# Kernel optimization log

Hardware: AMD Instinct MI355X
Metric: run time of the kernel (lower is better)

## Reference

```python
import jax, jax.numpy as jnp
import numpy as np
import math

B, T, D = 64, 128, 512
ALPHA = 20.0


def setup_inputs() -> dict:
    key = jax.random.key(0)
    k1, k2 = jax.random.split(key)
    x = jax.random.normal(k1, (B, T, D), dtype=jnp.float32)
    # Per-timestep fresh LSTMCell weights: uniform(-stdv, stdv) + tiled identity,
    # matching CellPro's re-initialization each step (stdv = 1/sqrt(1024)).
    stdv = 1.0 / math.sqrt(1024.0)
    eye4 = jnp.tile(jnp.eye(D, dtype=jnp.float32), (4, 1))  # [4D, D]
    w_ih = jax.random.uniform(k2, (T, 4 * D, D), dtype=jnp.float32,
                              minval=-stdv, maxval=stdv) + eye4[None]
    # Note: w_hh is also a parameter in the original, but h0 = 0 so it never
    # contributes to the output (gates = x @ w_ih^T + 0 @ w_hh^T). Omitted.
    return {"x": x, "w_ih": w_ih}


def reference(x, w_ih):
    # gates[b,t,:] = x[b,t,:] @ w_ih[t].T   (zero initial hidden state)
    gates = jnp.einsum('btd,tkd->btk', x, w_ih)  # [B, T, 4D]
    i, f, g, o = jnp.split(gates, 4, axis=-1)    # PyTorch LSTM gate order i,f,g,o
    c = jax.nn.sigmoid(i) * jnp.tanh(g)          # c' = f*c0 + i*g with c0 = 0
    h = jax.nn.sigmoid(o) * jnp.tanh(c)          # h' = o * tanh(c')
    return jax.nn.softmax(ALPHA * h, axis=-1)    # [B, T, D]
```

## Files before the change

kernel.cpp:

```cpp
#include <hip/hip_runtime.h>
#include <hip/hip_bf16.h>


#define B_ 64
#define T_ 128
#define D_ 512

typedef float f32x4_t __attribute__((ext_vector_type(4)));
typedef __bf16 bf16x8_t __attribute__((ext_vector_type(8)));
typedef unsigned short u16x8_t __attribute__((ext_vector_type(8)));
typedef unsigned short u16x4_t __attribute__((ext_vector_type(4)));

#define SWZ(r) ((unsigned)(((r) & 7) << 4))

__device__ __forceinline__ void cvt8(float4 a, float4 b, u16x8_t& hi, u16x8_t& lo) {
  float f[8] = {a.x, a.y, a.z, a.w, b.x, b.y, b.z, b.w};
#pragma unroll
  for (int j = 0; j < 8; ++j) {
    __bf16 h = (__bf16)f[j];
    hi[j] = __builtin_bit_cast(unsigned short, h);
    float r = f[j] - (float)h;
    lo[j] = __builtin_bit_cast(unsigned short, (__bf16)r);
  }
}

__device__ __forceinline__ void cvt4(float4 v, u16x4_t& hi, u16x4_t& lo) {
  float f[4] = {v.x, v.y, v.z, v.w};
#pragma unroll
  for (int j = 0; j < 4; ++j) {
    __bf16 h = (__bf16)f[j];
    hi[j] = __builtin_bit_cast(unsigned short, h);
    float r = f[j] - (float)h;
    lo[j] = __builtin_bit_cast(unsigned short, (__bf16)r);
  }
}

__device__ __forceinline__ f32x4_t mfma16(u16x8_t a, u16x8_t b, f32x4_t c) {
  return __builtin_amdgcn_mfma_f32_16x16x32_bf16(
      __builtin_bit_cast(bf16x8_t, a), __builtin_bit_cast(bf16x8_t, b), c, 0, 0, 0);
}

__device__ __forceinline__ float sigmoid_f(float v) { return 1.0f / (1.0f + __expf(-v)); }
__device__ __forceinline__ float tanh_f(float v) { return 1.0f - 2.0f / (__expf(2.0f * v) + 1.0f); }

__global__ __launch_bounds__(256, 2) void lstm_gates_kernel(
    const float* __restrict__ x, const float* __restrict__ w, float* __restrict__ out) {
  __shared__ char lds[2][16384];
  const int lane = threadIdx.x & 63;
  const int wv = threadIdx.x >> 6;
  const int bid = blockIdx.x;
  const int work = (bid & 7) * 128 + (bid >> 3);
  const int t = work >> 3;
  const int d0 = (work & 7) << 6;

  const int c = lane & 15;
  const int kg = lane >> 4;

  const int kl = lane * 4;
  const unsigned wst = (unsigned)(((kl >> 5) & 7) * 128);
  const unsigned wlow = (unsigned)((((kl >> 3) & 3) * 16) + ((kl & 4) << 1));
  unsigned wa_hi[4], wa_lo[4];
#pragma unroll
  for (int i = 0; i < 4; ++i) {
    const int rl = wv * 4 + i;
    wa_hi[i] = (unsigned)(rl * 1024) + wst + (wlow ^ SWZ(rl));
    wa_lo[i] = (unsigned)(rl * 1024) + wst + ((wlow + 64) ^ SWZ(rl));
  }
  const unsigned q_hi = ((unsigned)(kg * 16)) ^ SWZ(c);
  const unsigned q_lo = ((unsigned)(kg * 16 + 64)) ^ SWZ(c);
  const unsigned rbase = (unsigned)(c * 1024);

  const int grow[3] = {0, 1024, 1536};
  const char* wt = (const char*)w + ((size_t)t << 22) + (size_t)d0 * 2048;

  f32x4_t acc[12];
#pragma unroll
  for (int s = 0; s < 12; ++s) acc[s] = (f32x4_t){0.f, 0.f, 0.f, 0.f};

  u16x8_t xh[8], xl[8];
  float4 rs0[4], rs1[4];

#define LOADX(KH)                                                                      \
  do {                                                                                 \
    const float* xr_ = x + (((size_t)(wv * 16 + c) * T_ + t) << 9) + (KH) * 256 + kg * 8; \
    _Pragma("unroll") for (int st_ = 0; st_ < 8; ++st_) {                              \
      float4 a_ = *(const float4*)(xr_ + st_ * 32);                                    \
      float4 b_ = *(const float4*)(xr_ + st_ * 32 + 4);                                \
      cvt8(a_, b_, xh[st_], xl[st_]);                                                  \
    }                                                                                  \
  } while (0)

#define WOFF(SS)                                                                        \
  ((size_t)(grow[((SS) % 12) >> 2] + (((SS) % 12) & 3) * 16 + wv * 4) * 2048 +          \
   (size_t)((SS) / 12) * 1024)

#define ISSUE(SS, RS)                                                                   \
  do {                                                                                  \
    const char* gb_ = wt + WOFF(SS) + lane * 16;                                        \
    _Pragma("unroll") for (int i_ = 0; i_ < 4; ++i_)                                    \
        RS[i_] = *(const float4*)(gb_ + (size_t)i_ * 2048);                             \
  } while (0)

#define WRITE(SS, RS)                                                                   \
  do {                                                                                  \
    char* lb_ = &lds[(SS) & 1][0];                                                      \
    _Pragma("unroll") for (int i_ = 0; i_ < 4; ++i_) {                                  \
      u16x4_t h_, l_;                                                                   \
      cvt4(RS[i_], h_, l_);                                                             \
      *(u16x4_t*)(lb_ + wa_hi[i_]) = h_;                                                \
      *(u16x4_t*)(lb_ + wa_lo[i_]) = l_;                                                \
    }                                                                                   \
  } while (0)

#define BARRIER asm volatile("s_waitcnt lgkmcnt(0)\n\ts_barrier" ::: "memory")

#define COMPUTE(SS)                                                                     \
  do {                                                                                  \
    const char* lb_ = &lds[(SS) & 1][0];                                                \
    _Pragma("unroll") for (int st_ = 0; st_ < 8; ++st_) {                               \
      u16x8_t wh_ = *(const u16x8_t*)(lb_ + rbase + st_ * 128 + q_hi);                  \
      u16x8_t wl_ = *(const u16x8_t*)(lb_ + rbase + st_ * 128 + q_lo);                  \
      acc[(SS) % 12] = mfma16(xh[st_], wh_, acc[(SS) % 12]);                            \
      acc[(SS) % 12] = mfma16(xh[st_], wl_, acc[(SS) % 12]);                            \
      acc[(SS) % 12] = mfma16(xl[st_], wh_, acc[(SS) % 12]);                            \
    }                                                                                   \
  } while (0)

#define STEP(SS, RS)                        \
  WRITE(SS, RS);                            \
  if ((SS) + 2 < 24) ISSUE((SS) + 2, RS);   \
  BARRIER;                                  \
  COMPUTE(SS)

  LOADX(0);
  ISSUE(0, rs0);
  ISSUE(1, rs1);

  STEP(0, rs0);  STEP(1, rs1);  STEP(2, rs0);  STEP(3, rs1);
  STEP(4, rs0);  STEP(5, rs1);  STEP(6, rs0);  STEP(7, rs1);
  STEP(8, rs0);  STEP(9, rs1);  STEP(10, rs0); STEP(11, rs1);
  LOADX(1);
  STEP(12, rs0); STEP(13, rs1); STEP(14, rs0); STEP(15, rs1);
  STEP(16, rs0); STEP(17, rs1); STEP(18, rs0); STEP(19, rs1);
  STEP(20, rs0); STEP(21, rs1); STEP(22, rs0); STEP(23, rs1);

#undef STEP
#undef COMPUTE
#undef WRITE
#undef ISSUE
#undef WOFF
#undef LOADX

#pragma unroll
  for (int cg = 0; cg < 4; ++cg) {
#pragma unroll
    for (int j = 0; j < 4; ++j) {
      float iv = acc[cg][j];
      float gv = acc[4 + cg][j];
      float ov = acc[8 + cg][j];
      float cc = sigmoid_f(iv) * tanh_f(gv);
      float h = sigmoid_f(ov) * tanh_f(cc);
      int b = wv * 16 + kg * 4 + j;
      out[(((size_t)b * T_ + t) << 9) + d0 + cg * 16 + c] = h;
    }
  }
}

__global__ __launch_bounds__(256) void softmax_kernel(float* __restrict__ io) {
  const int lane = threadIdx.x & 63;
  const int row = blockIdx.x * 4 + (threadIdx.x >> 6);
  float* p = io + ((size_t)row << 9);
  float4 v0 = *(const float4*)(p + lane * 4);
  float4 v1 = *(const float4*)(p + 256 + lane * 4);
  float l[8] = {20.f * v0.x, 20.f * v0.y, 20.f * v0.z, 20.f * v0.w,
                20.f * v1.x, 20.f * v1.y, 20.f * v1.z, 20.f * v1.w};
  float m = l[0];
#pragma unroll
  for (int j = 1; j < 8; ++j) m = fmaxf(m, l[j]);
#pragma unroll
  for (int o = 32; o > 0; o >>= 1) m = fmaxf(m, __shfl_xor(m, o, 64));
  float e[8], s = 0.f;
#pragma unroll
  for (int j = 0; j < 8; ++j) {
    e[j] = __expf(l[j] - m);
    s += e[j];
  }
#pragma unroll
  for (int o = 32; o > 0; o >>= 1) s += __shfl_xor(s, o, 64);
  float inv = 1.0f / s;
  float4 o0 = {e[0] * inv, e[1] * inv, e[2] * inv, e[3] * inv};
  float4 o1 = {e[4] * inv, e[5] * inv, e[6] * inv, e[7] * inv};
  *(float4*)(p + lane * 4) = o0;
  *(float4*)(p + 256 + lane * 4) = o1;
}

extern "C" void kernel_launch(void* const* d_in, const int* in_sizes, int n_in,
                              void* d_out, int out_size, void* d_ws, size_t ws_size,
                              hipStream_t stream) {
  const float* x = (const float*)d_in[0];
  const float* w = (const float*)d_in[1];
  float* out = (float*)d_out;
  lstm_gates_kernel<<<T_ * 8, 256, 0, stream>>>(x, w, out);
  softmax_kernel<<<(B_ * T_) / 4, 256, 0, stream>>>(out);
}
```

Baseline: 98.37 us.

## Reorder K/gate loop to shrink accumulators from twelve to three

Changes the step order so that each column group's three gates (i, g, o) are accumulated over the full K before moving on. Only three accumulator tiles are live instead of twelve, and the epilogue runs and stores per column group. This lowers register pressure, which may help occupancy or avoid spills. In exchange, the x fragments are reloaded and reconverted from global memory eight times per block instead of twice, adding global loads and conversion ALU work.

```diff
diff --git a/kernel.cpp b/kernel.cpp
--- a/kernel.cpp
+++ b/kernel.cpp
@@ -73,57 +73,57 @@
   const int grow[3] = {0, 1024, 1536};
   const char* wt = (const char*)w + ((size_t)t << 22) + (size_t)d0 * 2048;
 
-  f32x4_t acc[12];
-#pragma unroll
-  for (int s = 0; s < 12; ++s) acc[s] = (f32x4_t){0.f, 0.f, 0.f, 0.f};
+  f32x4_t acc[3];
+#pragma unroll
+  for (int g = 0; g < 3; ++g) acc[g] = (f32x4_t){0.f, 0.f, 0.f, 0.f};
 
   u16x8_t xh[8], xl[8];
   float4 rs0[4], rs1[4];
 
-#define LOADX(KH)                                                                      \
-  do {                                                                                 \
+#define LOADX(KH)                                                                         \
+  do {                                                                                    \
     const float* xr_ = x + (((size_t)(wv * 16 + c) * T_ + t) << 9) + (KH) * 256 + kg * 8; \
-    _Pragma("unroll") for (int st_ = 0; st_ < 8; ++st_) {                              \
-      float4 a_ = *(const float4*)(xr_ + st_ * 32);                                    \
-      float4 b_ = *(const float4*)(xr_ + st_ * 32 + 4);                                \
-      cvt8(a_, b_, xh[st_], xl[st_]);                                                  \
-    }                                                                                  \
-  } while (0)
-
-#define WOFF(SS)                                                                        \
-  ((size_t)(grow[((SS) % 12) >> 2] + (((SS) % 12) & 3) * 16 + wv * 4) * 2048 +          \
-   (size_t)((SS) / 12) * 1024)
-
-#define ISSUE(SS, RS)                                                                   \
-  do {                                                                                  \
-    const char* gb_ = wt + WOFF(SS) + lane * 16;                                        \
-    _Pragma("unroll") for (int i_ = 0; i_ < 4; ++i_)                                    \
-        RS[i_] = *(const float4*)(gb_ + (size_t)i_ * 2048);                             \
-  } while (0)
-
-#define WRITE(SS, RS)                                                                   \
-  do {                                                                                  \
-    char* lb_ = &lds[(SS) & 1][0];                                                      \
-    _Pragma("unroll") for (int i_ = 0; i_ < 4; ++i_) {                                  \
-      u16x4_t h_, l_;                                                                   \
-      cvt4(RS[i_], h_, l_);                                                             \
-      *(u16x4_t*)(lb_ + wa_hi[i_]) = h_;                                                \
-      *(u16x4_t*)(lb_ + wa_lo[i_]) = l_;                                                \
-    }                                                                                   \
+    _Pragma("unroll") for (int st_ = 0; st_ < 8; ++st_) {                                 \
+      float4 a_ = *(const float4*)(xr_ + st_ * 32);                                       \
+      float4 b_ = *(const float4*)(xr_ + st_ * 32 + 4);                                   \
+      cvt8(a_, b_, xh[st_], xl[st_]);                                                     \
+    }                                                                                     \
+  } while (0)
+
+#define WOFF(SS)                                                                \
+  ((size_t)(grow[(SS) % 3] + ((SS) / 6) * 16 + wv * 4) * 2048 +                 \
+   (size_t)(((SS) / 3) & 1) * 1024)
+
+#define ISSUE(SS, RS)                                                           \
+  do {                                                                          \
+    const char* gb_ = wt + WOFF(SS) + lane * 16;                                \
+    _Pragma("unroll") for (int i_ = 0; i_ < 4; ++i_)                            \
+        RS[i_] = *(const float4*)(gb_ + (size_t)i_ * 2048);                     \
+  } while (0)
+
+#define WRITE(SS, RS)                                                           \
+  do {                                                                          \
+    char* lb_ = &lds[(SS) & 1][0];                                              \
+    _Pragma("unroll") for (int i_ = 0; i_ < 4; ++i_) {                          \
+      u16x4_t h_, l_;                                                           \
+      cvt4(RS[i_], h_, l_);                                                     \
+      *(u16x4_t*)(lb_ + wa_hi[i_]) = h_;                                        \
+      *(u16x4_t*)(lb_ + wa_lo[i_]) = l_;                                        \
+    }                                                                           \
   } while (0)
 
 #define BARRIER asm volatile("s_waitcnt lgkmcnt(0)\n\ts_barrier" ::: "memory")
 
-#define COMPUTE(SS)                                                                     \
-  do {                                                                                  \
-    const char* lb_ = &lds[(SS) & 1][0];                                                \
-    _Pragma("unroll") for (int st_ = 0; st_ < 8; ++st_) {                               \
-      u16x8_t wh_ = *(const u16x8_t*)(lb_ + rbase + st_ * 128 + q_hi);                  \
-      u16x8_t wl_ = *(const u16x8_t*)(lb_ + rbase + st_ * 128 + q_lo);                  \
-      acc[(SS) % 12] = mfma16(xh[st_], wh_, acc[(SS) % 12]);                            \
-      acc[(SS) % 12] = mfma16(xh[st_], wl_, acc[(SS) % 12]);                            \
-      acc[(SS) % 12] = mfma16(xl[st_], wh_, acc[(SS) % 12]);                            \
-    }                                                                                   \
+#define COMPUTE(SS)                                                             \
+  do {                                                                          \
+    const char* lb_ = &lds[(SS) & 1][0];                                        \
+    _Pragma("unroll") for (int st_ = 0; st_ < 8; ++st_) {                       \
+      u16x8_t wh_ = *(const u16x8_t*)(lb_ + rbase + st_ * 128 + q_hi);          \
+      u16x8_t wl_ = *(const u16x8_t*)(lb_ + rbase + st_ * 128 + q_lo);          \
+      acc[(SS) % 3] = mfma16(xh[st_], wh_, acc[(SS) % 3]);                      \
+      acc[(SS) % 3] = mfma16(xh[st_], wl_, acc[(SS) % 3]);                      \
+      acc[(SS) % 3] = mfma16(xl[st_], wh_, acc[(SS) % 3]);                      \
+    }                                                                           \
   } while (0)
 
 #define STEP(SS, RS)                        \
@@ -132,38 +132,42 @@
   BARRIER;                                  \
   COMPUTE(SS)
 
-  LOADX(0);
+#define EPILOG(CG)                                                              \
+  do {                                                                          \
+    _Pragma("unroll") for (int j_ = 0; j_ < 4; ++j_) {                          \
+      float iv_ = acc[0][j_], gv_ = acc[1][j_], ov_ = acc[2][j_];               \
+      float cc_ = sigmoid_f(iv_) * tanh_f(gv_);                                 \
+      float h_ = sigmoid_f(ov_) * tanh_f(cc_);                                  \
+      int b_ = wv * 16 + kg * 4 + j_;                                           \
+      out[(((size_t)b_ * T_ + t) << 9) + d0 + (CG) * 16 + c] = h_;              \
+    }                                                                           \
+    _Pragma("unroll") for (int g_ = 0; g_ < 3; ++g_)                            \
+        acc[g_] = (f32x4_t){0.f, 0.f, 0.f, 0.f};                                \
+  } while (0)
+
   ISSUE(0, rs0);
   ISSUE(1, rs1);
 
-  STEP(0, rs0);  STEP(1, rs1);  STEP(2, rs0);  STEP(3, rs1);
-  STEP(4, rs0);  STEP(5, rs1);  STEP(6, rs0);  STEP(7, rs1);
-  STEP(8, rs0);  STEP(9, rs1);  STEP(10, rs0); STEP(11, rs1);
-  LOADX(1);
-  STEP(12, rs0); STEP(13, rs1); STEP(14, rs0); STEP(15, rs1);
-  STEP(16, rs0); STEP(17, rs1); STEP(18, rs0); STEP(19, rs1);
-  STEP(20, rs0); STEP(21, rs1); STEP(22, rs0); STEP(23, rs1);
-
+  LOADX(0); STEP(0, rs0);  STEP(1, rs1);  STEP(2, rs0);
+  LOADX(1); STEP(3, rs1);  STEP(4, rs0);  STEP(5, rs1);
+  EPILOG(0);
+  LOADX(0); STEP(6, rs0);  STEP(7, rs1);  STEP(8, rs0);
+  LOADX(1); STEP(9, rs1);  STEP(10, rs0); STEP(11, rs1);
+  EPILOG(1);
+  LOADX(0); STEP(12, rs0); STEP(13, rs1); STEP(14, rs0);
+  LOADX(1); STEP(15, rs1); STEP(16, rs0); STEP(17, rs1);
+  EPILOG(2);
+  LOADX(0); STEP(18, rs0); STEP(19, rs1); STEP(20, rs0);
+  LOADX(1); STEP(21, rs1); STEP(22, rs0); STEP(23, rs1);
+  EPILOG(3);
+
+#undef EPILOG
 #undef STEP
 #undef COMPUTE
 #undef WRITE
 #undef ISSUE
 #undef WOFF
 #undef LOADX
-
-#pragma unroll
-  for (int cg = 0; cg < 4; ++cg) {
-#pragma unroll
-    for (int j = 0; j < 4; ++j) {
-      float iv = acc[cg][j];
-      float gv = acc[4 + cg][j];
-      float ov = acc[8 + cg][j];
-      float cc = sigmoid_f(iv) * tanh_f(gv);
-      float h = sigmoid_f(ov) * tanh_f(cc);
-      int b = wv * 16 + kg * 4 + j;
-      out[(((size_t)b * T_ + t) << 9) + d0 + cg * 16 + c] = h;
-    }
-  }
 }
 
 __global__ __launch_bounds__(256) void softmax_kernel(float* __restrict__ io) {
```

After: 123.5 us. +25.5%, slower.
